# Performance work log

Hardware: AMD Instinct MI355X
Metric: run time of the kernel (lower is better)

The kernel has to match this reference:

```python
import jax, jax.numpy as jnp
import numpy as np


def setup_inputs() -> dict:
    key = jax.random.key(0)
    k_q, k_k, k_v, k_xd, k_yd = jax.random.split(key, 5)
    B, L, H, E, K = 8, 4096, 2048, 512, 64
    return {
        "queries": jax.random.normal(k_q, (B, L, E), dtype=jnp.float32),
        "keys": jax.random.normal(k_k, (B, L, E), dtype=jnp.float32),
        "values": jax.random.normal(k_v, (B, L, E), dtype=jnp.float32),
        "x_date": jax.random.normal(k_xd, (B, L, K), dtype=jnp.float32),
        "y_date": jax.random.normal(k_yd, (B, H, K), dtype=jnp.float32),
    }


def reference(queries, keys, values, x_date, y_date):
    # queries/keys are unused in the original forward's math (only shapes).
    k = x_date.shape[-1]
    scale = 1.0 / float(np.sqrt(k))  # self.scale is None -> 1/sqrt(k)
    # scores: [B, L, H] from date features
    scores = jnp.einsum('blk,bhk->blh', x_date, y_date)
    # softmax over target axis H (dim=-1), numerically stable
    A = jax.nn.softmax(scale * scores, axis=-1)  # [B, L, H]
    # weighted reduction over source axis L -> [B, H, E]
    V = jnp.einsum('ble,blh->bhe', values, A)
    return V
```

## Files before the change

kernel.cpp:

```cpp
#include <hip/hip_runtime.h>
#include <hip/hip_bf16.h>

#define BN 8
#define LN 4096
#define HN 2048
#define EN 512
#define KN 64
#define LT 32
#define NIT 128

typedef __attribute__((ext_vector_type(8))) short bf16x8;
typedef __attribute__((ext_vector_type(4))) float f32x4;

__device__ __forceinline__ short f2b(float x) {
  union { float f; unsigned u; } v; v.f = x;
  unsigned r = v.u + 0x7fffu + ((v.u >> 16) & 1u);
  return (short)(r >> 16);
}

__device__ __forceinline__ bf16x8 cvt8(const float* __restrict__ p) {
  f32x4 a = *(const f32x4*)(p);
  f32x4 b = *(const f32x4*)(p + 4);
  bf16x8 r;
  r[0] = f2b(a[0]); r[1] = f2b(a[1]); r[2] = f2b(a[2]); r[3] = f2b(a[3]);
  r[4] = f2b(b[0]); r[5] = f2b(b[1]); r[6] = f2b(b[2]); r[7] = f2b(b[3]);
  return r;
}

__device__ __forceinline__ void gload16(const void* g, void* s) {
  __builtin_amdgcn_global_load_lds(
      (const __attribute__((address_space(1))) unsigned int*)(unsigned long long)g,
      (__attribute__((address_space(3))) unsigned int*)(unsigned int)(unsigned long long)s,
      16, 0, 0);
}

__global__ __launch_bounds__(256) void prep_cvt2(const float* __restrict__ xs,
                                                 short* __restrict__ xo,
                                                 const float* __restrict__ ys,
                                                 short* __restrict__ yo) {
  int bx = blockIdx.x;
  const float* src;
  short* dst;
  float scale;
  int i;
  if (bx < 1024) {
    i = bx * 256 + threadIdx.x;
    src = xs; dst = xo; scale = 0.125f * 1.4426950408889634f;
  } else {
    i = (bx - 1024) * 256 + threadIdx.x;
    src = ys; dst = yo; scale = 1.0f;
  }
  f32x4 a = *(const f32x4*)(src + (size_t)i * 8);
  f32x4 b = *(const f32x4*)(src + (size_t)i * 8 + 4);
  bf16x8 r;
  r[0] = f2b(a[0] * scale); r[1] = f2b(a[1] * scale);
  r[2] = f2b(a[2] * scale); r[3] = f2b(a[3] * scale);
  r[4] = f2b(b[0] * scale); r[5] = f2b(b[1] * scale);
  r[6] = f2b(b[2] * scale); r[7] = f2b(b[3] * scale);
  *(bf16x8*)(dst + (size_t)i * 8) = r;
}

__global__ __launch_bounds__(256) void k_pv_stats(const float* __restrict__ vals,
                                                  short* __restrict__ valsT,
                                                  const short* __restrict__ xb,
                                                  const short* __restrict__ yb,
                                                  float* __restrict__ ps) {
  __shared__ short tile[64 * 66];
  const int bx = blockIdx.x;
  const int tid = threadIdx.x;
  if (bx < 4096) {
    const int b = bx >> 9;
    const int e0 = ((bx >> 6) & 7) * 64;
    const int l0 = (bx & 63) * 64;
    {
      int lr = tid >> 2, ec = (tid & 3) * 16;
      const float* src = vals + ((size_t)b * LN + l0 + lr) * EN + e0 + ec;
      short* trow = tile + lr * 66 + ec;
#pragma unroll
      for (int q = 0; q < 4; ++q) {
        f32x4 v = *(const f32x4*)(src + q * 4);
        unsigned u0 = (unsigned)(unsigned short)f2b(v[0]) | ((unsigned)(unsigned short)f2b(v[1]) << 16);
        unsigned u1 = (unsigned)(unsigned short)f2b(v[2]) | ((unsigned)(unsigned short)f2b(v[3]) << 16);
        *(unsigned*)(trow + q * 4) = u0;
        *(unsigned*)(trow + q * 4 + 2) = u1;
      }
    }
    __syncthreads();
    {
      int er = tid >> 2, lc = (tid & 3) * 16;
      union { short s[16]; bf16x8 v[2]; } u;
#pragma unroll
      for (int k2 = 0; k2 < 16; ++k2) u.s[k2] = tile[(lc + k2) * 66 + er];
      short* dst = valsT + ((size_t)b * EN + e0 + er) * LN + l0 + lc;
      *(bf16x8*)dst = u.v[0];
      *(bf16x8*)(dst + 8) = u.v[1];
    }
  } else {
    const int idx = bx - 4096;
    const int b = (idx >> 5) & 7, hc = idx >> 8;
    const int w = tid >> 6, lane = tid & 63;
    const int row = lane & 15, g = lane >> 4;
    const int lb = (idx & 31) * 128 + w * 32;
    const size_t bL = (size_t)b * LN, bH = (size_t)b * HN;
    bf16x8 xa[2][2];
#pragma unroll
    for (int lt = 0; lt < 2; ++lt) {
      const short* xp = xb + ((bL + lb + lt * 16 + row) << 6) + 8 * g;
      xa[lt][0] = *(const bf16x8*)xp;
      xa[lt][1] = *(const bf16x8*)(xp + 32);
    }
    float s[2][4] = {{0.f, 0.f, 0.f, 0.f}, {0.f, 0.f, 0.f, 0.f}};
    const short* ybase = yb + ((bH + hc * 512 + row) << 6) + 8 * g;
#pragma unroll 2
    for (int it = 0; it < 32; ++it) {
      const short* yp = ybase + ((size_t)it << 10);
      bf16x8 y0 = *(const bf16x8*)yp;
      bf16x8 y1 = *(const bf16x8*)(yp + 32);
#pragma unroll
      for (int lt = 0; lt < 2; ++lt) {
        f32x4 a = {0.f, 0.f, 0.f, 0.f};
        a = __builtin_amdgcn_mfma_f32_16x16x32_bf16(xa[lt][0], y0, a, 0, 0, 0);
        a = __builtin_amdgcn_mfma_f32_16x16x32_bf16(xa[lt][1], y1, a, 0, 0, 0);
#pragma unroll
        for (int r = 0; r < 4; ++r) s[lt][r] += __builtin_amdgcn_exp2f(a[r]);
      }
    }
#pragma unroll
    for (int d = 1; d < 16; d <<= 1)
#pragma unroll
      for (int lt = 0; lt < 2; ++lt)
#pragma unroll
        for (int r = 0; r < 4; ++r) s[lt][r] += __shfl_xor(s[lt][r], d);
    if (row == 0) {
#pragma unroll
      for (int lt = 0; lt < 2; ++lt)
#pragma unroll
        for (int r = 0; r < 4; ++r)
          ps[(size_t)hc * (BN * LN) + bL + lb + lt * 16 + 4 * g + r] = s[lt][r];
    }
  }
}

__global__ void k_comb(const float* __restrict__ ps, float* __restrict__ wv) {
  int idx = blockIdx.x * 256 + threadIdx.x;
  float z = ps[idx] + ps[BN * LN + idx] + ps[2 * BN * LN + idx] + ps[3 * BN * LN + idx];
  wv[idx] = 1.0f / z;
}

__global__ __launch_bounds__(512, 4) void k_main3(
    const short* __restrict__ valsT, const short* __restrict__ xb,
    const short* __restrict__ yb, const float* __restrict__ wv,
    float* __restrict__ out) {
  __shared__ __align__(16) char smem[65920];
  const int tid = threadIdx.x;
  const int w = tid >> 6, lane = tid & 63;
  const int row = lane & 15, g = lane >> 4;

  const int f = blockIdx.x;
  const int b = f & 7;
  const int rest = f >> 3;
  const int hb = (rest & 31) * 64;
  const int eb = (rest >> 5) * 256;
  const size_t bL = (size_t)b * LN, bH = (size_t)b * HN;

  const int wbase = __builtin_amdgcn_readfirstlane(tid & ~63);

  const short* vsrc[2];
#pragma unroll
  for (int j = 0; j < 2; ++j) {
    int i = j * 512 + tid;
    int e = i >> 2, sl = (i & 3) ^ ((e >> 1) & 3);
    vsrc[j] = valsT + (((size_t)b * EN + eb + e) << 12) + 8 * sl;
  }
  const short* xsrc;
  {
    int p = w * 32 + (lane & 31);
    int l = p >> 3, sl = (p & 7) ^ (l & 7);
    xsrc = xb + ((bL + l) << 6) + 8 * sl;
  }
  const float* ssrc = wv + bL + 4 * tid;

  auto stage = [&](int buf, int tl) {
    int loff = tl * 32;
#pragma unroll
    for (int j = 0; j < 2; ++j)
      gload16(vsrc[j] + loff, smem + buf * 16384 + (j * 8192 + wbase * 16));
    if (lane < 32)
      gload16(xsrc + loff * 64, smem + 49152 + buf * 4096 + wbase * 8);
    if (tid < 8)
      gload16(ssrc + loff, smem + 65536 + buf * 128);
  };

  const int ht = w >> 1, lt = w & 1;
  bf16x8 ya0, ya1;
  {
    const short* yp = yb + ((bH + hb + ht * 16 + row) << 6) + 8 * g;
    ya0 = *(const bf16x8*)yp;
    ya1 = *(const bf16x8*)(yp + 32);
  }
  const int sp0 = g ^ (row & 7);
  const int xoffA = ((lt * 16 + row) << 7) + (sp0 << 4);
  const int xoffB = ((lt * 16 + row) << 7) + ((sp0 ^ 4) << 4);
  const int swoff = (lt * 16 + 4 * g) * 4;
  const int hq1 = ht * 16 + row;
  const int poff_w = hq1 * 64 + (((2 * lt + (g >> 1)) ^ ((hq1 >> 1) & 3)) << 4) + (g & 1) * 8;
  const int hq2a = (w >> 2) * 32 + row, hq2b = hq2a + 16;
  const int paoffA = hq2a * 64 + ((g ^ ((hq2a >> 1) & 3)) << 4);
  const int paoffB = hq2b * 64 + ((g ^ ((hq2b >> 1) & 3)) << 4);
  int vboff[4];
#pragma unroll
  for (int n = 0; n < 4; ++n) {
    int el = (w & 3) * 64 + n * 16 + row;
    vboff[n] = el * 64 + ((g ^ ((el >> 1) & 3)) << 4);
  }

  f32x4 acc[2][4];
#pragma unroll
  for (int at = 0; at < 2; ++at)
#pragma unroll
    for (int n = 0; n < 4; ++n) acc[at][n] = (f32x4){0.f, 0.f, 0.f, 0.f};

  stage(0, 0);
  stage(1, 1);
  asm volatile("s_waitcnt vmcnt(3)" ::: "memory");
  __builtin_amdgcn_s_barrier();
  asm volatile("" ::: "memory");

  int rb = 0, sb = 2;
  for (int it = 0; it < NIT; ++it) {
    if (it + 2 < NIT) stage(sb, it + 2);

    {
      const char* xbuf = smem + 49152 + rb * 4096;
      bf16x8 xa0 = *(const bf16x8*)(xbuf + xoffA);
      bf16x8 xa1 = *(const bf16x8*)(xbuf + xoffB);
      f32x4 sws = *(const f32x4*)(smem + 65536 + rb * 128 + swoff);
      f32x4 s4 = {0.f, 0.f, 0.f, 0.f};
      s4 = __builtin_amdgcn_mfma_f32_16x16x32_bf16(xa0, ya0, s4, 0, 0, 0);
      s4 = __builtin_amdgcn_mfma_f32_16x16x32_bf16(xa1, ya1, s4, 0, 0, 0);
      unsigned u0 = (unsigned)(unsigned short)f2b(__builtin_amdgcn_exp2f(s4[0]) * sws[0]) |
                    ((unsigned)(unsigned short)f2b(__builtin_amdgcn_exp2f(s4[1]) * sws[1]) << 16);
      unsigned u1 = (unsigned)(unsigned short)f2b(__builtin_amdgcn_exp2f(s4[2]) * sws[2]) |
                    ((unsigned)(unsigned short)f2b(__builtin_amdgcn_exp2f(s4[3]) * sws[3]) << 16);
      *(unsigned long long*)(smem + 61440 + poff_w) =
          (unsigned long long)u0 | ((unsigned long long)u1 << 32);
    }
    asm volatile("s_waitcnt lgkmcnt(0)" ::: "memory");
    __builtin_amdgcn_s_barrier();
    asm volatile("" ::: "memory");

    {
      const char* vbuf = smem + rb * 16384;
      bf16x8 pa0 = *(const bf16x8*)(smem + 61440 + paoffA);
      bf16x8 pa1 = *(const bf16x8*)(smem + 61440 + paoffB);
#pragma unroll
      for (int n = 0; n < 4; ++n) {
        bf16x8 vb = *(const bf16x8*)(vbuf + vboff[n]);
        acc[0][n] = __builtin_amdgcn_mfma_f32_16x16x32_bf16(pa0, vb, acc[0][n], 0, 0, 0);
        acc[1][n] = __builtin_amdgcn_mfma_f32_16x16x32_bf16(pa1, vb, acc[1][n], 0, 0, 0);
      }
    }
    if (it < NIT - 2)
      asm volatile("s_waitcnt vmcnt(3) lgkmcnt(0)" ::: "memory");
    else
      asm volatile("s_waitcnt vmcnt(0) lgkmcnt(0)" ::: "memory");
    __builtin_amdgcn_s_barrier();
    asm volatile("" ::: "memory");

    rb = rb == 2 ? 0 : rb + 1;
    sb = sb == 2 ? 0 : sb + 1;
  }

#pragma unroll
  for (int at = 0; at < 2; ++at)
#pragma unroll
    for (int n = 0; n < 4; ++n)
#pragma unroll
      for (int r = 0; r < 4; ++r) {
        int h = hb + (w >> 2) * 32 + at * 16 + 4 * g + r;
        int e = eb + (w & 3) * 64 + n * 16 + row;
        out[(bH + h) * (size_t)EN + e] = acc[at][n][r];
      }
}

__global__ __launch_bounds__(256) void k_stats_o(const float* __restrict__ xd,
                                                 const float* __restrict__ yd,
                                                 float* __restrict__ mz) {
  const int b = blockIdx.y;
  const int w = threadIdx.x >> 6;
  const int lane = threadIdx.x & 63;
  const int row = lane & 15, g = lane >> 4;
  const int lb = blockIdx.x * 64 + w * 16;
  const float* xp = xd + ((size_t)b * LN + lb + row) * KN + g * 8;
  bf16x8 a0 = cvt8(xp), a1 = cvt8(xp + 32);
  float m[4], s[4];
#pragma unroll
  for (int r = 0; r < 4; ++r) { m[r] = -1e30f; s[r] = 0.f; }
  const float* ybp = yd + ((size_t)b * HN + row) * KN + g * 8;
  for (int h0 = 0; h0 < HN; h0 += 16) {
    bf16x8 b0 = cvt8(ybp + (size_t)h0 * KN);
    bf16x8 b1 = cvt8(ybp + (size_t)h0 * KN + 32);
    f32x4 acc = {0.f, 0.f, 0.f, 0.f};
    acc = __builtin_amdgcn_mfma_f32_16x16x32_bf16(a0, b0, acc, 0, 0, 0);
    acc = __builtin_amdgcn_mfma_f32_16x16x32_bf16(a1, b1, acc, 0, 0, 0);
#pragma unroll
    for (int r = 0; r < 4; ++r) {
      float v = acc[r] * 0.125f;
      float mn = fmaxf(m[r], v);
      s[r] = s[r] * __expf(m[r] - mn) + __expf(v - mn);
      m[r] = mn;
    }
  }
#pragma unroll
  for (int d = 1; d < 16; d <<= 1) {
#pragma unroll
    for (int r = 0; r < 4; ++r) {
      float mo = __shfl_xor(m[r], d);
      float so = __shfl_xor(s[r], d);
      float mn = fmaxf(m[r], mo);
      s[r] = s[r] * __expf(m[r] - mn) + so * __expf(mo - mn);
      m[r] = mn;
    }
  }
  if (row == 0) {
#pragma unroll
    for (int r = 0; r < 4; ++r) {
      size_t idx = (size_t)b * LN + lb + 4 * g + r;
      mz[idx] = m[r];
      mz[(size_t)BN * LN + idx] = 1.0f / s[r];
    }
  }
}

__global__ __launch_bounds__(512) void k_main_o(const float* __restrict__ vals,
                                                const float* __restrict__ xd,
                                                const float* __restrict__ yd,
                                                const float* __restrict__ mz,
                                                float* __restrict__ out) {
  __shared__ short vT[256][34];
  __shared__ short pT[128][34];
  __shared__ short xT[LT][72];
  __shared__ float smm[LT], smz[LT];
  const int b = blockIdx.z;
  const int hb = blockIdx.x * 128;
  const int eb = blockIdx.y * 256;
  const int tid = threadIdx.x;
  const int w = tid >> 6, lane = tid & 63;
  const int row = lane & 15, g = lane >> 4;
  const float* yp = yd + ((size_t)b * HN + hb + w * 16 + row) * KN + g * 8;
  bf16x8 ya0 = cvt8(yp), ya1 = cvt8(yp + 32);
  f32x4 acc[16];
#pragma unroll
  for (int n = 0; n < 16; ++n) acc[n] = (f32x4){0.f, 0.f, 0.f, 0.f};
  const float* mzb = mz + (size_t)b * LN;
  const float* rzb = mz + (size_t)BN * LN + (size_t)b * LN;
  for (int l0 = 0; l0 < LN; l0 += LT) {
    __syncthreads();
    {
      int xl = tid >> 4, xk = (tid & 15) * 4;
      f32x4 xv = *(const f32x4*)(xd + ((size_t)b * LN + l0 + xl) * KN + xk);
      union { short h[4]; int i[2]; } u;
      u.h[0] = f2b(xv[0]); u.h[1] = f2b(xv[1]); u.h[2] = f2b(xv[2]); u.h[3] = f2b(xv[3]);
      int* dst = (int*)(&xT[xl][xk]);
      dst[0] = u.i[0]; dst[1] = u.i[1];
    }
#pragma unroll
    for (int lp = 0; lp < 4; ++lp) {
      int vl = (tid >> 6) + lp * 8;
      const float* vrow = vals + ((size_t)b * LN + l0 + vl) * EN + eb;
#pragma unroll
      for (int u2 = 0; u2 < 4; ++u2) {
        int e = (tid & 63) + u2 * 64;
        vT[e][vl] = f2b(vrow[e]);
      }
    }
    if (tid < LT) { smm[tid] = mzb[l0 + tid]; smz[tid] = rzb[l0 + tid]; }
    __syncthreads();
#pragma unroll
    for (int t2 = 0; t2 < 2; ++t2) {
      const short* xr = &xT[t2 * 16 + row][0];
      bf16x8 xb0 = *(const bf16x8*)(xr + 8 * g);
      bf16x8 xb1 = *(const bf16x8*)(xr + 32 + 8 * g);
      f32x4 sa = {0.f, 0.f, 0.f, 0.f};
      sa = __builtin_amdgcn_mfma_f32_16x16x32_bf16(ya0, xb0, sa, 0, 0, 0);
      sa = __builtin_amdgcn_mfma_f32_16x16x32_bf16(ya1, xb1, sa, 0, 0, 0);
      int lcol = t2 * 16 + row;
      float mm = smm[lcol], zz = smz[lcol];
#pragma unroll
      for (int r = 0; r < 4; ++r) {
        float p = __expf(sa[r] * 0.125f - mm) * zz;
        pT[w * 16 + 4 * g + r][lcol] = f2b(p);
      }
    }
    __syncthreads();
    bf16x8 pa;
    {
      const int* pi = (const int*)(&pT[w * 16 + row][0] + 8 * g);
      union { int i[4]; bf16x8 f; } u;
      u.i[0] = pi[0]; u.i[1] = pi[1]; u.i[2] = pi[2]; u.i[3] = pi[3];
      pa = u.f;
    }
#pragma unroll
    for (int n = 0; n < 16; ++n) {
      const int* vi = (const int*)(&vT[n * 16 + row][0] + 8 * g);
      union { int i[4]; bf16x8 f; } u;
      u.i[0] = vi[0]; u.i[1] = vi[1]; u.i[2] = vi[2]; u.i[3] = vi[3];
      acc[n] = __builtin_amdgcn_mfma_f32_16x16x32_bf16(pa, u.f, acc[n], 0, 0, 0);
    }
  }
#pragma unroll
  for (int n = 0; n < 16; ++n)
#pragma unroll
    for (int r = 0; r < 4; ++r) {
      int h = hb + w * 16 + 4 * g + r;
      int e = eb + n * 16 + row;
      out[((size_t)b * HN + h) * EN + e] = acc[n][r];
    }
}

extern "C" void kernel_launch(void* const* d_in, const int* in_sizes, int n_in,
                              void* d_out, int out_size, void* d_ws, size_t ws_size,
                              hipStream_t stream) {
  const float* vals = (const float*)d_in[2];
  const float* xd = (const float*)d_in[3];
  const float* yd = (const float*)d_in[4];
  float* out = (float*)d_out;

  if (ws_size >= 40501248ull) {
    char* wsb = (char*)d_ws;
    short* valsT = (short*)wsb;
    short* xbuf  = (short*)(wsb + 33554432);
    short* ybuf  = (short*)(wsb + 37748736);
    float* ps    = (float*)(wsb + 39845888);
    float* wv    = (float*)(wsb + 40370176);

    prep_cvt2<<<dim3(1536), 256, 0, stream>>>(xd, xbuf, yd, ybuf);
    k_pv_stats<<<dim3(5120), 256, 0, stream>>>(vals, valsT, xbuf, ybuf, ps);
    k_comb<<<dim3(BN * LN / 256), 256, 0, stream>>>(ps, wv);
    k_main3<<<dim3(512), 512, 0, stream>>>(valsT, xbuf, ybuf, wv, out);
  } else {
    float* mz = (float*)d_ws;
    k_stats_o<<<dim3(LN / 64, BN), 256, 0, stream>>>(xd, yd, mz);
    k_main_o<<<dim3(HN / 128, EN / 256, BN), 512, 0, stream>>>(vals, xd, yd, mz, out);
  }
}
```

Measured before the change: 182.2 us.

## Software-pipeline P production with double-buffered LDS and rework values transpose

The main kernel double-buffers the probability tile in LDS. Each iteration now produces the next tile's softmax weights while consuming the current one, which removes one barrier per iteration and gives the P·V MFMAs higher wave priority. Global loads are reordered so the x and weight loads issue before the values loads, and the vmcnt waits are adjusted to match. The values transpose kernel now packs pairs of L rows into dwords and uses an XOR-swizzled LDS layout, so it can do wide 16-byte LDS reads in place of scalar short gathers. This uses more LDS, which may affect occupancy.

```diff
diff --git a/kernel.cpp b/kernel.cpp
--- a/kernel.cpp
+++ b/kernel.cpp
@@ -11,6 +11,7 @@
 
 typedef __attribute__((ext_vector_type(8))) short bf16x8;
 typedef __attribute__((ext_vector_type(4))) float f32x4;
+typedef __attribute__((ext_vector_type(4))) unsigned u32x4;
 
 __device__ __forceinline__ short f2b(float x) {
   union { float f; unsigned u; } v; v.f = x;
@@ -65,7 +66,7 @@
                                                   const short* __restrict__ xb,
                                                   const short* __restrict__ yb,
                                                   float* __restrict__ ps) {
-  __shared__ short tile[64 * 66];
+  __shared__ unsigned trT[2048];
   const int bx = blockIdx.x;
   const int tid = threadIdx.x;
   if (bx < 4096) {
@@ -73,27 +74,33 @@
     const int e0 = ((bx >> 6) & 7) * 64;
     const int l0 = (bx & 63) * 64;
     {
-      int lr = tid >> 2, ec = (tid & 3) * 16;
-      const float* src = vals + ((size_t)b * LN + l0 + lr) * EN + e0 + ec;
-      short* trow = tile + lr * 66 + ec;
-#pragma unroll
-      for (int q = 0; q < 4; ++q) {
-        f32x4 v = *(const f32x4*)(src + q * 4);
-        unsigned u0 = (unsigned)(unsigned short)f2b(v[0]) | ((unsigned)(unsigned short)f2b(v[1]) << 16);
-        unsigned u1 = (unsigned)(unsigned short)f2b(v[2]) | ((unsigned)(unsigned short)f2b(v[3]) << 16);
-        *(unsigned*)(trow + q * 4) = u0;
-        *(unsigned*)(trow + q * 4 + 2) = u1;
+      int lr2 = tid >> 3;
+      int ec = (tid & 7) * 8;
+      const float* r0 = vals + ((size_t)b * LN + l0 + 2 * lr2) * EN + e0 + ec;
+      const float* r1 = r0 + EN;
+      f32x4 a0 = *(const f32x4*)r0, a1 = *(const f32x4*)(r0 + 4);
+      f32x4 c0 = *(const f32x4*)r1, c1 = *(const f32x4*)(r1 + 4);
+#pragma unroll
+      for (int j = 0; j < 8; ++j) {
+        float lo = (j < 4) ? a0[j] : a1[j - 4];
+        float hi = (j < 4) ? c0[j] : c1[j - 4];
+        unsigned dw = (unsigned)(unsigned short)f2b(lo) |
+                      ((unsigned)(unsigned short)f2b(hi) << 16);
+        int e = ec + j;
+        int sz = (((e >> 3) ^ e) & 7) << 2;
+        trT[e * 32 + (lr2 ^ sz)] = dw;
       }
     }
     __syncthreads();
     {
-      int er = tid >> 2, lc = (tid & 3) * 16;
-      union { short s[16]; bf16x8 v[2]; } u;
-#pragma unroll
-      for (int k2 = 0; k2 < 16; ++k2) u.s[k2] = tile[(lc + k2) * 66 + er];
-      short* dst = valsT + ((size_t)b * EN + e0 + er) * LN + l0 + lc;
-      *(bf16x8*)dst = u.v[0];
-      *(bf16x8*)(dst + 8) = u.v[1];
+      int er = tid >> 2, lq = (tid & 3) * 8;
+      int sr = ((er >> 3) ^ er) & 7;
+      const unsigned* base = trT + er * 32;
+      u32x4 u0 = *(const u32x4*)(base + ((((lq >> 2) + 0) ^ sr) << 2));
+      u32x4 u1 = *(const u32x4*)(base + ((((lq >> 2) + 1) ^ sr) << 2));
+      short* dst = valsT + ((size_t)b * EN + e0 + er) * LN + l0 + 2 * lq;
+      *(u32x4*)dst = u0;
+      *(u32x4*)(dst + 8) = u1;
     }
   } else {
     const int idx = bx - 4096;
@@ -147,11 +154,11 @@
   wv[idx] = 1.0f / z;
 }
 
-__global__ __launch_bounds__(512, 4) void k_main3(
+__global__ __launch_bounds__(512, 4) void k_main4(
     const short* __restrict__ valsT, const short* __restrict__ xb,
     const short* __restrict__ yb, const float* __restrict__ wv,
     float* __restrict__ out) {
-  __shared__ __align__(16) char smem[65920];
+  __shared__ __align__(16) char smem[70016];
   const int tid = threadIdx.x;
   const int w = tid >> 6, lane = tid & 63;
   const int row = lane & 15, g = lane >> 4;
@@ -182,13 +189,13 @@
 
   auto stage = [&](int buf, int tl) {
     int loff = tl * 32;
-#pragma unroll
-    for (int j = 0; j < 2; ++j)
-      gload16(vsrc[j] + loff, smem + buf * 16384 + (j * 8192 + wbase * 16));
     if (lane < 32)
       gload16(xsrc + loff * 64, smem + 49152 + buf * 4096 + wbase * 8);
     if (tid < 8)
-      gload16(ssrc + loff, smem + 65536 + buf * 128);
+      gload16(ssrc + loff, smem + 69632 + buf * 128);
+#pragma unroll
+    for (int j = 0; j < 2; ++j)
+      gload16(vsrc[j] + loff, smem + buf * 16384 + (j * 8192 + wbase * 16));
   };
 
   const int ht = w >> 1, lt = w & 1;
@@ -220,56 +227,61 @@
 #pragma unroll
     for (int n = 0; n < 4; ++n) acc[at][n] = (f32x4){0.f, 0.f, 0.f, 0.f};
 
+  auto produce = [&](int bx1, int pp) {
+    const char* xbuf = smem + 49152 + bx1 * 4096;
+    bf16x8 xa0 = *(const bf16x8*)(xbuf + xoffA);
+    bf16x8 xa1 = *(const bf16x8*)(xbuf + xoffB);
+    f32x4 sws = *(const f32x4*)(smem + 69632 + bx1 * 128 + swoff);
+    f32x4 s4 = {0.f, 0.f, 0.f, 0.f};
+    s4 = __builtin_amdgcn_mfma_f32_16x16x32_bf16(xa0, ya0, s4, 0, 0, 0);
+    s4 = __builtin_amdgcn_mfma_f32_16x16x32_bf16(xa1, ya1, s4, 0, 0, 0);
+    unsigned u0 = (unsigned)(unsigned short)f2b(__builtin_amdgcn_exp2f(s4[0]) * sws[0]) |
+                  ((unsigned)(unsigned short)f2b(__builtin_amdgcn_exp2f(s4[1]) * sws[1]) << 16);
+    unsigned u1 = (unsigned)(unsigned short)f2b(__builtin_amdgcn_exp2f(s4[2]) * sws[2]) |
+                  ((unsigned)(unsigned short)f2b(__builtin_amdgcn_exp2f(s4[3]) * sws[3]) << 16);
+    *(unsigned long long*)(smem + 61440 + pp * 4096 + poff_w) =
+        (unsigned long long)u0 | ((unsigned long long)u1 << 32);
+  };
+
+  auto consume = [&](int rbv, int pp) {
+    const char* vbuf = smem + rbv * 16384;
+    const char* pbuf = smem + 61440 + pp * 4096;
+    bf16x8 pa0 = *(const bf16x8*)(pbuf + paoffA);
+    bf16x8 pa1 = *(const bf16x8*)(pbuf + paoffB);
+    __builtin_amdgcn_s_setprio(1);
+#pragma unroll
+    for (int n = 0; n < 4; ++n) {
+      bf16x8 vb = *(const bf16x8*)(vbuf + vboff[n]);
+      acc[0][n] = __builtin_amdgcn_mfma_f32_16x16x32_bf16(pa0, vb, acc[0][n], 0, 0, 0);
+      acc[1][n] = __builtin_amdgcn_mfma_f32_16x16x32_bf16(pa1, vb, acc[1][n], 0, 0, 0);
+    }
+    __builtin_amdgcn_s_setprio(0);
+  };
+
   stage(0, 0);
   stage(1, 1);
-  asm volatile("s_waitcnt vmcnt(3)" ::: "memory");
+  asm volatile("s_waitcnt vmcnt(2)" ::: "memory");
   __builtin_amdgcn_s_barrier();
-  asm volatile("" ::: "memory");
-
-  int rb = 0, sb = 2;
-  for (int it = 0; it < NIT; ++it) {
-    if (it + 2 < NIT) stage(sb, it + 2);
-
-    {
-      const char* xbuf = smem + 49152 + rb * 4096;
-      bf16x8 xa0 = *(const bf16x8*)(xbuf + xoffA);
-      bf16x8 xa1 = *(const bf16x8*)(xbuf + xoffB);
-      f32x4 sws = *(const f32x4*)(smem + 65536 + rb * 128 + swoff);
-      f32x4 s4 = {0.f, 0.f, 0.f, 0.f};
-      s4 = __builtin_amdgcn_mfma_f32_16x16x32_bf16(xa0, ya0, s4, 0, 0, 0);
-      s4 = __builtin_amdgcn_mfma_f32_16x16x32_bf16(xa1, ya1, s4, 0, 0, 0);
-      unsigned u0 = (unsigned)(unsigned short)f2b(__builtin_amdgcn_exp2f(s4[0]) * sws[0]) |
-                    ((unsigned)(unsigned short)f2b(__builtin_amdgcn_exp2f(s4[1]) * sws[1]) << 16);
-      unsigned u1 = (unsigned)(unsigned short)f2b(__builtin_amdgcn_exp2f(s4[2]) * sws[2]) |
-                    ((unsigned)(unsigned short)f2b(__builtin_amdgcn_exp2f(s4[3]) * sws[3]) << 16);
-      *(unsigned long long*)(smem + 61440 + poff_w) =
-          (unsigned long long)u0 | ((unsigned long long)u1 << 32);
-    }
-    asm volatile("s_waitcnt lgkmcnt(0)" ::: "memory");
-    __builtin_amdgcn_s_barrier();
-    asm volatile("" ::: "memory");
-
-    {
-      const char* vbuf = smem + rb * 16384;
-      bf16x8 pa0 = *(const bf16x8*)(smem + 61440 + paoffA);
-      bf16x8 pa1 = *(const bf16x8*)(smem + 61440 + paoffB);
-#pragma unroll
-      for (int n = 0; n < 4; ++n) {
-        bf16x8 vb = *(const bf16x8*)(vbuf + vboff[n]);
-        acc[0][n] = __builtin_amdgcn_mfma_f32_16x16x32_bf16(pa0, vb, acc[0][n], 0, 0, 0);
-        acc[1][n] = __builtin_amdgcn_mfma_f32_16x16x32_bf16(pa1, vb, acc[1][n], 0, 0, 0);
-      }
-    }
+  produce(0, 0);
+  asm volatile("s_waitcnt lgkmcnt(0)" ::: "memory");
+  __builtin_amdgcn_s_barrier();
+
+  int rbv = 0, bx1 = 1, sb = 2, p = 0;
+  for (int it = 0; it < NIT - 1; ++it) {
+    if (it < NIT - 2) stage(sb, it + 2);
+    produce(bx1, p ^ 1);
+    consume(rbv, p);
     if (it < NIT - 2)
-      asm volatile("s_waitcnt vmcnt(3) lgkmcnt(0)" ::: "memory");
+      asm volatile("s_waitcnt vmcnt(2) lgkmcnt(0)" ::: "memory");
     else
       asm volatile("s_waitcnt vmcnt(0) lgkmcnt(0)" ::: "memory");
     __builtin_amdgcn_s_barrier();
-    asm volatile("" ::: "memory");
-
-    rb = rb == 2 ? 0 : rb + 1;
+    rbv = rbv == 2 ? 0 : rbv + 1;
+    bx1 = bx1 == 2 ? 0 : bx1 + 1;
     sb = sb == 2 ? 0 : sb + 1;
-  }
+    p ^= 1;
+  }
+  consume(rbv, p);
 
 #pragma unroll
   for (int at = 0; at < 2; ++at)
@@ -388,8 +400,8 @@
       float mm = smm[lcol], zz = smz[lcol];
 #pragma unroll
       for (int r = 0; r < 4; ++r) {
-        float p = __expf(sa[r] * 0.125f - mm) * zz;
-        pT[w * 16 + 4 * g + r][lcol] = f2b(p);
+        float p2 = __expf(sa[r] * 0.125f - mm) * zz;
+        pT[w * 16 + 4 * g + r][lcol] = f2b(p2);
       }
     }
     __syncthreads();
@@ -437,7 +449,7 @@
     prep_cvt2<<<dim3(1536), 256, 0, stream>>>(xd, xbuf, yd, ybuf);
     k_pv_stats<<<dim3(5120), 256, 0, stream>>>(vals, valsT, xbuf, ybuf, ps);
     k_comb<<<dim3(BN * LN / 256), 256, 0, stream>>>(ps, wv);
-    k_main3<<<dim3(512), 512, 0, stream>>>(valsT, xbuf, ybuf, wv, out);
+    k_main4<<<dim3(512), 512, 0, stream>>>(valsT, xbuf, ybuf, wv, out);
   } else {
     float* mz = (float*)d_ws;
     k_stats_o<<<dim3(LN / 64, BN), 256, 0, stream>>>(xd, yd, mz);
```

Result: faster. 171.7 us (-5.8%).
